# Kernel optimization log

Hardware: AMD Instinct MI355X
Metric: run time of the kernel (lower is better)

## Reference

```python
import jax, jax.numpy as jnp
import numpy as np


def setup_inputs() -> dict:
    key = jax.random.key(0)
    k1, k2 = jax.random.split(key)
    B, N, D = 32, 1024, 384
    x = jax.random.normal(k1, (B, N, D), dtype=jnp.float32)
    durations = jax.random.randint(k2, (B, N), 0, 8, dtype=jnp.int32)
    return {"x": x, "durations": durations, "max_len": 4096}


def reference(x, durations, max_len):
    # x: (B, N, D) encoder output; durations: (B, N) frames per phoneme.
    # Fused length-regulation: for each output frame t, source phoneme index is
    # the smallest n with cumsum(durations)[n] > t (searchsorted right on cumsum).
    B, N, D = x.shape
    cum = jnp.cumsum(durations, axis=1)              # (B, N)
    total = cum[:, -1]                               # (B,) total frames per row
    t = jnp.arange(max_len, dtype=cum.dtype)         # (T,)
    # (B, T) source index per output frame
    idx = jax.vmap(lambda c: jnp.searchsorted(c, t, side="right"))(cum)
    mel_mask = t[None, :] >= total[:, None]          # (B, T) True where padding
    idx_c = jnp.minimum(idx, N - 1)                  # clamp out-of-range (padded frames)
    out = jnp.take_along_axis(x, idx_c[:, :, None], axis=1)   # (B, T, D)
    out = jnp.where(mel_mask[:, :, None], jnp.zeros((), x.dtype), out)
    return out, mel_mask
```

## Files before the change

### kernel.cpp

```cpp
#include <hip/hip_runtime.h>

#define BB 32
#define NN 1024
#define DD 384
#define ML 4096
#define D4 (DD / 4)
#define ROWS 4
#define GT (ROWS * D4)

__global__ __launch_bounds__(NN) void lr_cumsum_kernel(
    const int* __restrict__ dur, int* __restrict__ cum) {
    __shared__ int s[NN];
    const int b = blockIdx.x;
    const int i = threadIdx.x;
    s[i] = dur[b * NN + i];
    __syncthreads();
    #pragma unroll
    for (int off = 1; off < NN; off <<= 1) {
        int v = (i >= off) ? s[i - off] : 0;
        __syncthreads();
        s[i] += v;
        __syncthreads();
    }
    cum[b * NN + i] = s[i];
}

__global__ __launch_bounds__(GT) void lr_gather_kernel(
    const float4* __restrict__ x, const int* __restrict__ cum,
    float4* __restrict__ out, float* __restrict__ mask) {
    __shared__ int sidx[ROWS];
    const int tid  = threadIdx.x;
    const int row0 = blockIdx.x * ROWS;

    if (tid < ROWS) {
        const int row = row0 + tid;
        const int b = row >> 12;
        const int t = row & (ML - 1);
        const int* __restrict__ c = cum + (b << 10);
        const int total = c[NN - 1];
        int pidx;
        if (t >= total) {
            pidx = -1;
        } else {
            int lo = 0, hi = NN;
            while (lo < hi) {
                const int mid = (lo + hi) >> 1;
                if (c[mid] > t) hi = mid; else lo = mid + 1;
            }
            pidx = lo;
        }
        sidx[tid] = pidx;
        mask[row] = (pidx < 0) ? 1.0f : 0.0f;
    }
    __syncthreads();

    const int r   = tid / D4;
    const int d4  = tid - r * D4;
    const int row = row0 + r;
    const int pidx = sidx[r];
    float4 v = {0.0f, 0.0f, 0.0f, 0.0f};
    if (pidx >= 0) {
        const int b = row >> 12;
        v = x[((b << 10) + pidx) * D4 + d4];
    }
    out[row * D4 + d4] = v;
}

extern "C" void kernel_launch(void* const* d_in, const int* in_sizes, int n_in,
                              void* d_out, int out_size, void* d_ws, size_t ws_size,
                              hipStream_t stream) {
    const float* x  = (const float*)d_in[0];
    const int* dur  = (const int*)d_in[1];

    int* cum    = (int*)d_ws;
    float* out  = (float*)d_out;
    float* mask = out + (size_t)BB * ML * DD;

    lr_cumsum_kernel<<<BB, NN, 0, stream>>>(dur, cum);
    lr_gather_kernel<<<(BB * ML) / ROWS, GT, 0, stream>>>(
        (const float4*)x, cum, (float4*)out, mask);
}
```

Before: 298.9 us.

## Scatter frame indices in scan kernel, replacing per-row binary search in gather

The scan kernel now writes each phoneme's index directly into its output frames in LDS, then emits a per-frame index array and the mask. This removes the serial binary search that a few threads ran in every gather block. The copy kernel loops three times over 8 rows per 256-thread block with a swizzled block order, and drops the shared-memory sync. The scan kernel now does serial scatter loops of up to 7 iterations per thread and one extra write and read of the index buffer.

```diff
diff --git a/kernel.cpp b/kernel.cpp
--- a/kernel.cpp
+++ b/kernel.cpp
@@ -5,16 +5,23 @@
 #define DD 384
 #define ML 4096
 #define D4 (DD / 4)
-#define ROWS 4
-#define GT (ROWS * D4)
+#define RPB 8
+#define GT2 256
+#define NBLK2 (BB * ML / RPB)
 
-__global__ __launch_bounds__(NN) void lr_cumsum_kernel(
-    const int* __restrict__ dur, int* __restrict__ cum) {
+__global__ __launch_bounds__(NN) void lr_scan_scatter_kernel(
+    const int* __restrict__ dur, int* __restrict__ idxb,
+    float* __restrict__ mask) {
     __shared__ int s[NN];
+    __shared__ int idx_lds[ML];
     const int b = blockIdx.x;
     const int i = threadIdx.x;
+
     s[i] = dur[b * NN + i];
+    #pragma unroll
+    for (int k = 0; k < ML / NN; ++k) idx_lds[i + k * NN] = -1;
     __syncthreads();
+
     #pragma unroll
     for (int off = 1; off < NN; off <<= 1) {
         int v = (i >= off) ? s[i - off] : 0;
@@ -22,61 +29,56 @@
         s[i] += v;
         __syncthreads();
     }
-    cum[b * NN + i] = s[i];
+
+    const int end_raw = s[i];
+    const int start   = (i == 0) ? 0 : s[i - 1];
+    const int end     = (end_raw < ML) ? end_raw : ML;
+    for (int t = start; t < end; ++t) idx_lds[t] = i;
+    __syncthreads();
+
+    #pragma unroll
+    for (int k = 0; k < ML / NN; ++k) {
+        const int t = i + k * NN;
+        const int v = idx_lds[t];
+        idxb[b * ML + t] = v;
+        mask[b * ML + t] = (v < 0) ? 1.0f : 0.0f;
+    }
 }
 
-__global__ __launch_bounds__(GT) void lr_gather_kernel(
-    const float4* __restrict__ x, const int* __restrict__ cum,
-    float4* __restrict__ out, float* __restrict__ mask) {
-    __shared__ int sidx[ROWS];
-    const int tid  = threadIdx.x;
-    const int row0 = blockIdx.x * ROWS;
+__global__ __launch_bounds__(GT2) void lr_copy_kernel(
+    const float4* __restrict__ x, const int* __restrict__ idxb,
+    float4* __restrict__ out) {
+    const int g = ((blockIdx.x & 7) * (NBLK2 / 8)) + (blockIdx.x >> 3);
+    const int row0 = g * RPB;
+    const int tid = threadIdx.x;
 
-    if (tid < ROWS) {
-        const int row = row0 + tid;
-        const int b = row >> 12;
-        const int t = row & (ML - 1);
-        const int* __restrict__ c = cum + (b << 10);
-        const int total = c[NN - 1];
-        int pidx;
-        if (t >= total) {
-            pidx = -1;
-        } else {
-            int lo = 0, hi = NN;
-            while (lo < hi) {
-                const int mid = (lo + hi) >> 1;
-                if (c[mid] > t) hi = mid; else lo = mid + 1;
-            }
-            pidx = lo;
+    #pragma unroll
+    for (int k = 0; k < 3; ++k) {
+        const int pos = tid + k * GT2;
+        const int r   = pos / D4;
+        const int d4  = pos - r * D4;
+        const int row = row0 + r;
+        const int idx = idxb[row];
+        float4 v = {0.0f, 0.0f, 0.0f, 0.0f};
+        if (idx >= 0) {
+            const int b = row >> 12;
+            v = x[((b << 10) + idx) * D4 + d4];
         }
-        sidx[tid] = pidx;
-        mask[row] = (pidx < 0) ? 1.0f : 0.0f;
+        out[(size_t)row * D4 + d4] = v;
     }
-    __syncthreads();
-
-    const int r   = tid / D4;
-    const int d4  = tid - r * D4;
-    const int row = row0 + r;
-    const int pidx = sidx[r];
-    float4 v = {0.0f, 0.0f, 0.0f, 0.0f};
-    if (pidx >= 0) {
-        const int b = row >> 12;
-        v = x[((b << 10) + pidx) * D4 + d4];
-    }
-    out[row * D4 + d4] = v;
 }
 
 extern "C" void kernel_launch(void* const* d_in, const int* in_sizes, int n_in,
                               void* d_out, int out_size, void* d_ws, size_t ws_size,
                               hipStream_t stream) {
-    const float* x  = (const float*)d_in[0];
-    const int* dur  = (const int*)d_in[1];
+    const float* x = (const float*)d_in[0];
+    const int* dur = (const int*)d_in[1];
 
-    int* cum    = (int*)d_ws;
+    int* idxb   = (int*)d_ws;
     float* out  = (float*)d_out;
     float* mask = out + (size_t)BB * ML * DD;
 
-    lr_cumsum_kernel<<<BB, NN, 0, stream>>>(dur, cum);
-    lr_gather_kernel<<<(BB * ML) / ROWS, GT, 0, stream>>>(
-        (const float4*)x, cum, (float4*)out, mask);
+    lr_scan_scatter_kernel<<<BB, NN, 0, stream>>>(dur, idxb, mask);
+    lr_copy_kernel<<<NBLK2, GT2, 0, stream>>>(
+        (const float4*)x, idxb, (float4*)out);
 }
```

After: 244.7 us. -18.1%, faster.
